# Performance work log

Measured on AMD Instinct MI355X. Metric: run time of the kernel, lower is better.

The kernel has to match this reference:

```python
import jax, jax.numpy as jnp
import numpy as np

N, C, K, KEIG, B, NG, H = 32768, 128, 5, 128, 64, 512, 4
E = 524288
EPS = 1e-5


def setup_inputs() -> dict:
    key = jax.random.key(0)
    ks = iter(jax.random.split(key, 40))
    def nrm(shape, scale):
        return jax.random.normal(next(ks), shape, jnp.float32) * scale
    s = 1.0 / np.sqrt(C)
    return dict(
        x=nrm((N, C), 1.0),
        U=nrm((N, KEIG), 1.0 / np.sqrt(N)),
        Lambda=jax.random.uniform(next(ks), (KEIG,), jnp.float32, 0.0, 2.0),
        lambda_max=jnp.full((1,), 2.0, jnp.float32),
        w_spa1=nrm((C, C), s), b_spa1=jnp.zeros((C,), jnp.float32),
        w_spa2=nrm((C, C), s), b_spa2=jnp.zeros((C,), jnp.float32),
        w_spe1=nrm((C, C), s), b_spe1=jnp.zeros((C,), jnp.float32),
        w_spe2=nrm((C, C), s), b_spe2=jnp.zeros((C,), jnp.float32),
        cheb_w=nrm((K, C, C), s), cheb_b=jnp.zeros((C,), jnp.float32),
        gamma=jnp.ones((1,), jnp.float32),
        w_proj=nrm((C, C), s),
        w_qkv=nrm((C, 3 * C), s), b_qkv=jnp.zeros((3 * C,), jnp.float32),
        w_out=nrm((C, C), s), b_out=jnp.zeros((C,), jnp.float32),
        mlp_w1=nrm((C, 2 * C), s), mlp_b1=jnp.zeros((2 * C,), jnp.float32),
        mlp_w2=nrm((2 * C, C), 1.0 / np.sqrt(2 * C)), mlp_b2=jnp.zeros((C,), jnp.float32),
        bn1_w=jnp.ones((C,), jnp.float32), bn1_b=jnp.zeros((C,), jnp.float32),
        bn2_w=jnp.ones((C,), jnp.float32), bn2_b=jnp.zeros((C,), jnp.float32),
        bn3_w=jnp.ones((C,), jnp.float32), bn3_b=jnp.zeros((C,), jnp.float32),
        edge_index=jax.random.randint(next(ks), (2, E), 0, N, jnp.int64) if jax.config.jax_enable_x64 else jax.random.randint(next(ks), (2, E), 0, N, jnp.int32),
        batch=jnp.repeat(jnp.arange(B), NG),  # 64 graphs of 512 nodes each
    )


def _mlp2(h, w1, b1, w2, b2):
    return jnp.maximum(h @ w1 + b1, 0.0) @ w2 + b2


def _bn(h, w, b):
    # train-mode BatchNorm1d over node dim (biased variance), GPSConv default norm
    mu = h.mean(0)
    var = jnp.mean((h - mu) ** 2, 0)
    return (h - mu) * jax.lax.rsqrt(var + EPS) * w + b


def _cheb(x, src, dst, lam, Ws, bias):
    # L_hat = (2/lambda_max) * (I - D^{-1/2} A D^{-1/2}) - I ; sym normalization
    deg = jax.ops.segment_sum(jnp.ones_like(src, x.dtype), src, num_segments=N)
    dis = jnp.where(deg > 0, 1.0 / jnp.sqrt(deg), 0.0)
    w = dis[src] * dis[dst]  # [E]
    scale = 2.0 / lam
    def lhat(v):
        agg = jax.ops.segment_sum(w[:, None] * v[src], dst, num_segments=N)
        return (scale - 1.0) * v - scale * agg
    Tx0 = x
    out = Tx0 @ Ws[0]
    Tx1 = lhat(Tx0)
    out = out + Tx1 @ Ws[1]
    for k in range(2, K):
        Tx2 = 2.0 * lhat(Tx1) - Tx0
        out = out + Tx2 @ Ws[k]
        Tx0, Tx1 = Tx1, Tx2
    return out + bias


def _mha(xd, w_qkv, b_qkv, w_out, b_out):
    Bq, n, _ = xd.shape
    dh = C // H
    qkv = xd @ w_qkv + b_qkv  # [B,n,3C]
    q, k, v = jnp.split(qkv, 3, axis=-1)
    heads = lambda t: t.reshape(Bq, n, H, dh).transpose(0, 2, 1, 3)
    q, k, v = heads(q), heads(k), heads(v)
    a = jax.nn.softmax(jnp.einsum('bhqd,bhkd->bhqk', q, k) / np.sqrt(dh), axis=-1)
    o = jnp.einsum('bhqk,bhkd->bhqd', a, v).transpose(0, 2, 1, 3).reshape(Bq, n, C)
    return o @ w_out + b_out


def reference(x, U, Lambda, lambda_max,
              w_spa1, b_spa1, w_spa2, b_spa2,
              w_spe1, b_spe1, w_spe2, b_spe2,
              cheb_w, cheb_b, gamma, w_proj,
              w_qkv, b_qkv, w_out, b_out,
              mlp_w1, mlp_b1, mlp_w2, mlp_b2,
              bn1_w, bn1_b, bn2_w, bn2_b, bn3_w, bn3_b,
              edge_index, batch):
    src, dst = edge_index[0], edge_index[1]
    lam = lambda_max[0]
    # ---- SpectralLocalNN (GPSConv local conv branch) ----
    x_sp = _mlp2(x, w_spa1, b_spa1, w_spa2, b_spa2)
    out_local = _cheb(x_sp, src, dst, lam, cheb_w, cheb_b)
    x_spec = _mlp2(x, w_spe1, b_spe1, w_spe2, b_spe2)
    h_proj = x_spec @ w_proj
    s_lam = jnp.exp(-gamma[0] * Lambda ** 2)  # [k_eig]
    out_spectral = U @ (s_lam[:, None] * (U.T @ h_proj))
    h1 = _bn(out_local + out_spectral + x, bn1_w, bn1_b)
    # ---- global attention branch (equal-size graphs -> dense reshape) ----
    xd = x.reshape(B, NG, C)
    h2 = _mha(xd, w_qkv, b_qkv, w_out, b_out).reshape(N, C)
    h2 = _bn(h2 + x, bn2_w, bn2_b)
    # ---- combine + MLP ----
    out = h1 + h2
    out = out + _mlp2(out, mlp_w1, mlp_b1, mlp_w2, mlp_b2)
    return _bn(out, bn3_w, bn3_b)
```

## Files before the change

### kernel.cpp

```cpp
#include <hip/hip_runtime.h>

typedef short bf16x8 __attribute__((ext_vector_type(8)));
typedef short bf16x4 __attribute__((ext_vector_type(4)));
typedef float f32x4 __attribute__((ext_vector_type(4)));

#define DEVI __device__ __forceinline__

constexpr int N   = 32768;
constexpr int C   = 128;
constexpr int E   = 524288;
constexpr float EPSV = 1e-5f;
constexpr int UT_BLOCKS = 128;
constexpr int HB  = 64;
constexpr int EPB = E / HB;
constexpr float QSCALE = 0.17677669529663687f * 1.4426950408889634f;

DEVI float bf2f(ushort u){ return __uint_as_float(((uint)u) << 16); }
DEVI ushort f2bf(float f){
  uint u = __float_as_uint(f);
  return (ushort)((u + 0x7fffu + ((u >> 16) & 1u)) >> 16);
}
DEVI uint cvtpk(float lo, float hi){
  uint r;
  asm("v_cvt_pk_bf16_f32 %0, %1, %2" : "=v"(r) : "v"(lo), "v"(hi));
  return r;
}
DEVI float fexp2(float x){
  float r;
  asm("v_exp_f32 %0, %1" : "=v"(r) : "v"(x));
  return r;
}
DEVI float sane(float v){ if (!(v == v)) return 0.f; return fminf(fmaxf(v, -1e30f), 1e30f); }
DEVI bool mode_fp32(const uint* lmraw){ return (lmraw[0] & 0xffffu) == 0u; }

constexpr int CSZ[28] = {128,1,16384,128,16384,128,16384,128,16384,128,81920,128,
                         1,16384,49152,384,16384,128,32768,256,32768,128,
                         128,128,128,128,128,128};
constexpr int COF[28] = {0,128,192,16576,16704,33088,33216,49600,49728,66112,
                         66240,148160,148288,148352,164736,213888,214272,230656,
                         230784,263552,263808,296576,296704,296832,296960,297088,
                         297216,297344};
constexpr int CAN_SMALL_TOTAL = 297472;

struct CvtArgs { const void* src[28]; };

__global__ __launch_bounds__(256) void convert_small(CvtArgs a, ushort* __restrict__ can,
                                                     const uint* __restrict__ lmraw)
{
  bool f32 = mode_fp32(lmraw);
  int idx = blockIdx.x * 256 + threadIdx.x;
  #pragma unroll 1
  for (int s = 0; s < 28; s++) {
    if (idx < CSZ[s]) {
      ushort v = f32 ? f2bf(((const float*)a.src[s])[idx])
                     : ((const ushort*)a.src[s])[idx];
      can[COF[s] + idx] = v;
      return;
    }
    idx -= CSZ[s];
  }
}

__global__ __launch_bounds__(256) void convert_big(const void* __restrict__ xs,
    const void* __restrict__ Us, ushort* __restrict__ canx, ushort* __restrict__ canu,
    const uint* __restrict__ lmraw)
{
  bool f32 = mode_fp32(lmraw);
  size_t e = ((size_t)blockIdx.x * 256 + threadIdx.x) * 4;
  bool isU = e >= (size_t)N * C;
  size_t off = isU ? e - (size_t)N * C : e;
  const void* src = isU ? Us : xs;
  ushort* dst = isU ? canu : canx;
  ushort4 o;
  if (f32) {
    float4 v = *(const float4*)((const float*)src + off);
    o.x = f2bf(v.x); o.y = f2bf(v.y); o.z = f2bf(v.z); o.w = f2bf(v.w);
  } else {
    o = *(const ushort4*)((const ushort*)src + off);
  }
  *(ushort4*)(dst + off) = o;
}

__global__ __launch_bounds__(1024) void hist_lds(const int* __restrict__ ei,
    int* __restrict__ cei, ushort* __restrict__ part)
{
  __shared__ uint hist[N / 2];
  int t = threadIdx.x;
  int b = blockIdx.x;
  bool i64 = ((ei[1] | ei[3] | ei[5] | ei[7]) == 0);
  size_t j0 = (size_t)b * EPB;
  #pragma unroll
  for (int i = t; i < N / 2; i += 1024) hist[i] = 0u;
  __syncthreads();
  for (int k = t; k < EPB; k += 1024) {
    size_t j = j0 + k;
    int v = (i64 ? ei[2 * j] : ei[j]) & (N - 1);
    cei[j] = v;
    atomicAdd(&hist[v >> 1], 1u << ((v & 1) * 16));
  }
  __syncthreads();
  uint* po = (uint*)(part + (size_t)b * N);
  for (int i = t; i < N / 2; i += 1024) po[i] = hist[i];
}

__global__ __launch_bounds__(256) void reduce_cnt(const ushort* __restrict__ part,
    int* __restrict__ cdt, float* __restrict__ dis)
{
  int d = blockIdx.x * 256 + threadIdx.x;
  int s = 0, tt = 0;
  #pragma unroll 8
  for (int b = 0; b < HB; b++) s  += part[(size_t)b * N + d];
  #pragma unroll 8
  for (int b = 0; b < HB; b++) tt += part[(size_t)(HB + b) * N + d];
  cdt[d] = tt;
  dis[d] = s > 0 ? rsqrtf((float)s) : 0.f;
}

__global__ __launch_bounds__(1024) void scan_kernel(const int* __restrict__ cnt,
                                                    int* __restrict__ row_ptr)
{
  __shared__ int sums[1024];
  int t = threadIdx.x;
  int loc[32]; int s = 0;
  int base = t * 32;
  #pragma unroll
  for (int i = 0; i < 32; i++) { loc[i] = s; s += cnt[base + i]; }
  sums[t] = s;
  __syncthreads();
  for (int off = 1; off < 1024; off <<= 1) {
    int v = (t >= off) ? sums[t - off] : 0;
    __syncthreads();
    sums[t] += v;
    __syncthreads();
  }
  int pre = (t == 0) ? 0 : sums[t - 1];
  #pragma unroll
  for (int i = 0; i < 32; i++) row_ptr[base + i] = pre + loc[i];
}

__global__ __launch_bounds__(256) void off_kernel(const int* __restrict__ rp,
    const ushort* __restrict__ part, int* __restrict__ off2)
{
  int d = blockIdx.x * 256 + threadIdx.x;
  int run = rp[d];
  #pragma unroll 8
  for (int b = 0; b < HB; b++) {
    off2[(size_t)b * N + d] = run;
    run += part[(size_t)(HB + b) * N + d];
  }
}

__global__ __launch_bounds__(1024) void edge_scatter(const int* __restrict__ cei,
    const int* __restrict__ off2, const float* __restrict__ dis,
    int2* __restrict__ ep)
{
  __shared__ int base[N];
  int t = threadIdx.x;
  int b = blockIdx.x;
  for (int i = t; i < N; i += 1024) base[i] = off2[(size_t)b * N + i];
  __syncthreads();
  size_t e0 = (size_t)b * EPB;
  for (int k = t; k < EPB; k += 1024) {
    size_t e = e0 + k;
    int s = cei[e], d = cei[e + E];
    int slot = atomicAdd(&base[d], 1);
    int2 v; v.x = s; v.y = __float_as_int(dis[s] * dis[d]);
    ep[slot] = v;
  }
}

constexpr int WT_SPA1 = 0;
constexpr int WT_SPA2 = 16384;
constexpr int WT_SPE1 = 32768;
constexpr int WT_SPE2 = 49152;
constexpr int WT_PROJ = 65536;
constexpr int WT_CHEB = 81920;
constexpr int WT_QKV  = 163840;
constexpr int WT_WOUT = 212992;
constexpr int WT_MLP1 = 229376;
constexpr int WT_MLP2 = 262144;
constexpr int WT_TOTAL = 294912;

__global__ __launch_bounds__(256) void zero_kernel(int* __restrict__ p, int n)
{
  int i = blockIdx.x * 256 + threadIdx.x;
  if (i < n) p[i] = 0;
}

__global__ __launch_bounds__(256) void transpose_weights(
    const ushort* __restrict__ spa1, const ushort* __restrict__ spa2,
    const ushort* __restrict__ spe1, const ushort* __restrict__ spe2,
    const ushort* __restrict__ proj, const ushort* __restrict__ cheb,
    const ushort* __restrict__ qkv,  const ushort* __restrict__ wout,
    const ushort* __restrict__ mlp1, const ushort* __restrict__ mlp2,
    ushort* __restrict__ wt)
{
  int i = blockIdx.x * 256 + threadIdx.x;
  if (i < 81920) {
    int m = i >> 14, r = i & 16383; int k = r >> 7, n = r & 127;
    const ushort* src = m==0?spa1 : m==1?spa2 : m==2?spe1 : m==3?spe2 : proj;
    wt[m*16384 + n*128 + k] = src[r];
  } else if (i < 163840) {
    int j = i - 81920; int m = j >> 14, r = j & 16383; int k = r >> 7, n = r & 127;
    wt[WT_CHEB + n*640 + m*128 + k] = cheb[j];
  } else if (i < 212992) {
    int j = i - 163840; int k = j / 384, n = j % 384;
    wt[WT_QKV + n*128 + k] = qkv[j];
  } else if (i < 229376) {
    int j = i - 212992; int k = j >> 7, n = j & 127;
    wt[WT_WOUT + n*128 + k] = wout[j];
  } else if (i < 262144) {
    int j = i - 229376; int k = j >> 8, n = j & 255;
    wt[WT_MLP1 + n*128 + k] = mlp1[j];
  } else if (i < WT_TOTAL) {
    int j = i - 262144; int k = j >> 7, n = j & 127;
    wt[WT_MLP2 + n*256 + k] = mlp2[j];
  }
}

template<int K, int COLS, bool RELU, int OMODE, bool BIAS, bool RES, int ASTR, int OSTR, bool QSC>
__global__ __launch_bounds__(256) void gemm_lds(
    const ushort* __restrict__ A, const ushort* __restrict__ WT,
    const ushort* __restrict__ bias, const ushort* __restrict__ res,
    void* __restrict__ outp)
{
  constexpr int NSEG = COLS / 128;
  constexpr int NKC = K / 128;
  constexpr int BP = 136;
  __shared__ ushort Bs[128 * BP];
  int tid = threadIdx.x;
  int lane = tid & 63, wave = tid >> 6;
  int quad = lane >> 4, l16 = lane & 15;
  int seg = (NSEG > 1) ? (blockIdx.x % NSEG) : 0;
  int rb  = (NSEG > 1) ? (blockIdx.x / NSEG) : blockIdx.x;
  int row0 = rb * 64 + wave * 16;
  const ushort* wseg = WT + (size_t)(seg * 128) * K;

  f32x4 acc[8];
  #pragma unroll
  for (int nt = 0; nt < 8; nt++) acc[nt] = (f32x4){0.f, 0.f, 0.f, 0.f};

  for (int kc = 0; kc < NKC; kc++) {
    if (kc) __syncthreads();
    #pragma unroll
    for (int i = tid; i < 2048; i += 256) {
      int col = i >> 4, ko = (i & 15) * 8;
      *(bf16x8*)&Bs[col * BP + ko] =
          *(const bf16x8*)(wseg + (size_t)col * K + kc * 128 + ko);
    }
    __syncthreads();
    bf16x8 a[4];
    const ushort* ap = A + (size_t)(row0 + l16) * ASTR + kc * 128 + quad * 8;
    #pragma unroll
    for (int kk = 0; kk < 4; kk++) a[kk] = *(const bf16x8*)(ap + kk * 32);
    #pragma unroll
    for (int kk = 0; kk < 4; kk++) {
      #pragma unroll
      for (int nt = 0; nt < 8; nt++) {
        bf16x8 b = *(const bf16x8*)(&Bs[(nt * 16 + l16) * BP + kk * 32 + quad * 8]);
        acc[nt] = __builtin_amdgcn_mfma_f32_16x16x32_bf16(a[kk], b, acc[nt], 0, 0, 0);
      }
    }
  }

  #pragma unroll
  for (int nt = 0; nt < 8; nt++) {
    int col = seg * 128 + nt * 16 + l16;
    float bv = 0.f;
    if (BIAS) bv = bf2f(bias[col]);
// ... 165 lines not shown
      #pragma unroll
      for (int nt = 0; nt < 8; nt++) {
        bf16x8 b = *(const bf16x8*)(&Bs[(nt * 16 + l16) * BP + kk * 32 + quad * 8]);
        acc[nt] = __builtin_amdgcn_mfma_f32_16x16x32_bf16(a[kk], b, acc[nt], 0, 0, 0);
      }
    #pragma unroll
    for (int nt = 0; nt < 8; nt++) {
      int col = seg * 128 + nt * 16 + l16;
      float bv = bf2f(B1[col]);
      #pragma unroll
      for (int r = 0; r < 4; r++)
        Hs[(lw + quad * 4 + r) * HP + col] = f2bf(fmaxf(acc[nt][r] + bv, 0.f));
    }
  }
  __syncthreads();

  f32x4 acc2[8];
  #pragma unroll
  for (int nt = 0; nt < 8; nt++) acc2[nt] = (f32x4){0.f, 0.f, 0.f, 0.f};
  for (int kc = 0; kc < 2; kc++) {
    if (kc) __syncthreads();
    for (int i = tid; i < 2048; i += 256) {
      int col = i >> 4, ko = (i & 15) * 8;
      *(bf16x8*)&Bs[col * BP + ko] =
          *(const bf16x8*)(W2 + (size_t)col * 256 + kc * 128 + ko);
    }
    bf16x8 a2[4];
    #pragma unroll
    for (int kk = 0; kk < 4; kk++)
      a2[kk] = *(const bf16x8*)(&Hs[(lw + l16) * HP + kc * 128 + kk * 32 + quad * 8]);
    __syncthreads();
    #pragma unroll
    for (int kk = 0; kk < 4; kk++)
      #pragma unroll
      for (int nt = 0; nt < 8; nt++) {
        bf16x8 b = *(const bf16x8*)(&Bs[(nt * 16 + l16) * BP + kk * 32 + quad * 8]);
        acc2[nt] = __builtin_amdgcn_mfma_f32_16x16x32_bf16(a2[kk], b, acc2[nt], 0, 0, 0);
      }
  }

  #pragma unroll
  for (int nt = 0; nt < 8; nt++) {
    int col = nt * 16 + l16;
    float bv = bf2f(B2[col]);
    #pragma unroll
    for (int r = 0; r < 4; r++) {
      int row = row0 + quad * 4 + r;
      float v = acc2[nt][r] + bv + bf2f(res[(size_t)row * 128 + col]);
      outp[(size_t)row * 128 + col] = v;
    }
  }
}

__global__ __launch_bounds__(256) void spmm_cheb(
    const int* __restrict__ row_ptr, const int2* __restrict__ ep,
    const ushort* __restrict__ v,
    const ushort* __restrict__ txprev, ushort* __restrict__ txout,
    const ushort* __restrict__ lambda_max, int first, int str)
{
  int wave = threadIdx.x >> 6, lane = threadIdx.x & 63;
  int sub = lane >> 4, l16 = lane & 15;
  int d = blockIdx.x * 4 + wave;
  float lm = bf2f(lambda_max[0]);
  float scale = 2.f / lm;
  if (!(scale == scale) || fabsf(scale) > 1e6f) scale = 1.f;
  int beg = row_ptr[d];
  int end = (d == N - 1) ? E : row_ptr[d + 1];
  float acc[8] = {0.f,0.f,0.f,0.f,0.f,0.f,0.f,0.f};
  for (int jb = beg; jb < end; jb += 4) {
    int j = jb + sub;
    bool ok = j < end;
    int2 e2 = ep[ok ? j : beg];
    int s = e2.x & (N - 1);
    float w = ok ? __int_as_float(e2.y) : 0.f;
    bf16x8 vv = *(const bf16x8*)(v + (size_t)s * str + l16 * 8);
    #pragma unroll
    for (int i = 0; i < 8; i++) acc[i] += w * bf2f((ushort)vv[i]);
  }
  #pragma unroll
  for (int i = 0; i < 8; i++) {
    acc[i] += __shfl_xor(acc[i], 16);
    acc[i] += __shfl_xor(acc[i], 32);
  }
  if (sub == 0) {
    bf16x8 vd = *(const bf16x8*)(v + (size_t)d * str + l16 * 8);
    bf16x8 tp;
    if (!first) tp = *(const bf16x8*)(txprev + (size_t)d * str + l16 * 8);
    bf16x8 ov;
    #pragma unroll
    for (int i = 0; i < 8; i++) {
      float r = (scale - 1.f) * bf2f((ushort)vd[i]) - scale * acc[i];
      if (!first) r = 2.f * r - bf2f((ushort)tp[i]);
      ov[i] = (short)f2bf(r);
    }
    *(bf16x8*)(txout + (size_t)d * str + l16 * 8) = ov;
  }
}

__global__ __launch_bounds__(256) void ut_mfma(const ushort* __restrict__ U,
    const ushort* __restrict__ hp, float* __restrict__ parts)
{
  constexpr int RP = 40;
  __shared__ ushort Ut[128 * RP];
  __shared__ ushort Ht[128 * RP];
  int t = threadIdx.x;
  int lane = t & 63, wave = t >> 6;
  int quad = lane >> 4, l16 = lane & 15;

  f32x4 acc[2][8];
  #pragma unroll
  for (int a = 0; a < 2; a++)
    #pragma unroll
    for (int ct = 0; ct < 8; ct++) acc[a][ct] = (f32x4){0.f, 0.f, 0.f, 0.f};

  for (int ch = 0; ch < 8; ch++) {
    int n0 = blockIdx.x * 256 + ch * 32;
    __syncthreads();
    for (int i = t; i < 2048; i += 256) {
      int r2 = i >> 7, c = i & 127;
      uint u0 = U [(size_t)(n0 + r2 * 2) * 128 + c];
      uint u1 = U [(size_t)(n0 + r2 * 2 + 1) * 128 + c];
      *(uint*)&Ut[c * RP + r2 * 2] = (u0 & 0xffffu) | (u1 << 16);
      uint h0 = hp[(size_t)(n0 + r2 * 2) * 128 + c];
      uint h1 = hp[(size_t)(n0 + r2 * 2 + 1) * 128 + c];
      *(uint*)&Ht[c * RP + r2 * 2] = (h0 & 0xffffu) | (h1 << 16);
    }
    __syncthreads();
    bf16x8 bfr[8];
    #pragma unroll
    for (int ct = 0; ct < 8; ct++)
      bfr[ct] = *(const bf16x8*)(&Ht[(ct * 16 + l16) * RP + quad * 8]);
    #pragma unroll
    for (int a = 0; a < 2; a++) {
      int kt = wave * 2 + a;
      bf16x8 af = *(const bf16x8*)(&Ut[(kt * 16 + l16) * RP + quad * 8]);
      #pragma unroll
      for (int ct = 0; ct < 8; ct++)
        acc[a][ct] = __builtin_amdgcn_mfma_f32_16x16x32_bf16(af, bfr[ct], acc[a][ct], 0, 0, 0);
    }
  }

  float* po = parts + (size_t)blockIdx.x * 16384;
  #pragma unroll
  for (int a = 0; a < 2; a++) {
    int kt = wave * 2 + a;
    #pragma unroll
    for (int ct = 0; ct < 8; ct++)
      #pragma unroll
      for (int r = 0; r < 4; r++)
        po[(kt * 16 + quad * 4 + r) * 128 + ct * 16 + l16] = acc[a][ct][r];
  }
}

__global__ __launch_bounds__(256) void reduce_mt(const float* __restrict__ parts,
    const ushort* __restrict__ Lambda, const ushort* __restrict__ gamma,
    ushort* __restrict__ MT)
{
  int e = blockIdx.x * 256 + threadIdx.x;
  int keig = e >> 7, c = e & 127;
  float s = 0.f;
  for (int p = 0; p < UT_BLOCKS; p++) s += parts[(size_t)p * 16384 + e];
  float g = bf2f(gamma[0]);
  float lam = bf2f(Lambda[keig]);
  float sl = __expf(-g * lam * lam);
  MT[c * 128 + keig] = f2bf(sl * s);
}

__global__ __launch_bounds__(256) void bn_stats(const float* __restrict__ h,
                                                float* __restrict__ stats)
{
  int c = threadIdx.x & 127, half = threadIdx.x >> 7;
  int r0 = blockIdx.x * 128 + half;
  float s = 0.f, s2 = 0.f;
  for (int i = 0; i < 64; i++) {
    float v = sane(h[(size_t)(r0 + i * 2) * 128 + c]);
    s += v; s2 += v * v;
  }
  atomicAdd(&stats[c], s);
  atomicAdd(&stats[128 + c], s2);
}

__global__ __launch_bounds__(256) void bn_apply(const float* __restrict__ h,
    const float* __restrict__ st, const ushort* __restrict__ gw,
    const ushort* __restrict__ gb, const ushort* __restrict__ add,
    void* __restrict__ out, const uint* __restrict__ lmraw, int final_out)
{
  size_t e = ((size_t)blockIdx.x * 256 + threadIdx.x) * 4;
  int c0 = (int)(e & 127);
  float4 hv = *(const float4*)(h + e);
  float xv[4] = {sane(hv.x), sane(hv.y), sane(hv.z), sane(hv.w)};
  float addv[4] = {0.f, 0.f, 0.f, 0.f};
  if (add) {
    ushort4 av = *(const ushort4*)(add + e);
    addv[0] = bf2f(av.x); addv[1] = bf2f(av.y);
    addv[2] = bf2f(av.z); addv[3] = bf2f(av.w);
  }
  float r[4];
  #pragma unroll
  for (int j = 0; j < 4; j++) {
    int c = c0 + j;
    float mu = st[c] * (1.f / 32768.f);
    float var = fmaxf(st[128 + c] * (1.f / 32768.f) - mu * mu, 0.f);
    r[j] = (xv[j] - mu) * rsqrtf(var + EPSV) * bf2f(gw[c]) + bf2f(gb[c]) + addv[j];
  }
  if (final_out && mode_fp32(lmraw)) {
    float4 o4; o4.x = r[0]; o4.y = r[1]; o4.z = r[2]; o4.w = r[3];
    *(float4*)((float*)out + e) = o4;
  } else {
    ushort4 o;
    o.x = f2bf(r[0]); o.y = f2bf(r[1]); o.z = f2bf(r[2]); o.w = f2bf(r[3]);
    *(ushort4*)((ushort*)out + e) = o;
  }
}

__global__ __launch_bounds__(512) void attn_mfma(const ushort* __restrict__ qkv,
                                                 ushort* __restrict__ attn)
{
  constexpr int VP = 516;
  constexpr int KP = 40;
  __shared__ ushort Kt[512 * KP];
  __shared__ ushort Vt[32 * VP];
  int b = blockIdx.x;
  int g = b >> 3, hh = (b >> 1) & 3, half = b & 1;
  int lane = threadIdx.x & 63, wave = threadIdx.x >> 6;
  int quad = lane >> 4, l16 = lane & 15;
  const ushort* base = qkv + (size_t)g * 512 * 384;

  for (int i = threadIdx.x; i < 512 * 4; i += 512) {
    int key = i >> 2, c8 = (i & 3) * 8;
    *(bf16x8*)&Kt[key * KP + c8] =
        *(const bf16x8*)(base + (size_t)key * 384 + 128 + hh * 32 + c8);
  }
  for (int i = threadIdx.x; i < 256 * 8; i += 512) {
    int kp = i >> 3, d4 = (i & 7) * 4;
    const ushort* va = base + (size_t)(2 * kp) * 384 + 256 + hh * 32 + d4;
    ushort4 a = *(const ushort4*)va;
    ushort4 c = *(const ushort4*)(va + 384);
    *(uint*)&Vt[(d4 + 0) * VP + 2 * kp] = (uint)a.x | ((uint)c.x << 16);
    *(uint*)&Vt[(d4 + 1) * VP + 2 * kp] = (uint)a.y | ((uint)c.y << 16);
    *(uint*)&Vt[(d4 + 2) * VP + 2 * kp] = (uint)a.z | ((uint)c.z << 16);
    *(uint*)&Vt[(d4 + 3) * VP + 2 * kp] = (uint)a.w | ((uint)c.w << 16);
  }
  __syncthreads();

  int q0 = half * 256 + wave * 32;
  bf16x8 qf[2];
  #pragma unroll
  for (int i = 0; i < 2; i++)
    qf[i] = *(const bf16x8*)(base + (size_t)(q0 + i * 16 + l16) * 384 + hh * 32 + quad * 8);

  f32x4 O[2][2];
  #pragma unroll
  for (int dt = 0; dt < 2; dt++)
    #pragma unroll
    for (int i = 0; i < 2; i++) O[dt][i] = (f32x4){0.f, 0.f, 0.f, 0.f};
  float lsum[2] = {0.f, 0.f};

  union PU { uint u[4]; bf16x8 v; };
  union VU { uint2 a[2]; bf16x8 v; };

  for (int kt2 = 0; kt2 < 16; kt2++) {
    int k0 = kt2 * 32;
    bf16x8 kfA = *(const bf16x8*)&Kt[(k0 + l16) * KP + quad * 8];
    bf16x8 kfB = *(const bf16x8*)&Kt[(k0 + 16 + l16) * KP + quad * 8];
// ... 68 lines not shown
constexpr size_t OFF_PARTS = 87 * MB;

extern "C" void kernel_launch(void* const* d_in, const int* in_sizes, int n_in,
                              void* d_out, int out_size, void* d_ws, size_t ws_size,
                              hipStream_t stream) {
  (void)in_sizes; (void)n_in; (void)out_size; (void)ws_size;
  const uint* lmraw = (const uint*)d_in[3];
  const int*  ei    = (const int*)d_in[30];

  char* W = (char*)d_ws;
  ushort* wt    = (ushort*)(W + OFF_WT);
  int*    cdt   = (int*)(W + OFF_CDT);
  int*    rp    = (int*)(W + OFF_RP);
  float*  dis   = (float*)(W + OFF_DIS);
  ushort* MT    = (ushort*)(W + OFF_MT);
  float*  stats = (float*)(W + OFF_STATS);
  int*    cei   = (int*)(W + OFF_CEI);
  int2*   ep    = (int2*)(W + OFF_EP);
  ushort* part  = (ushort*)(W + OFF_PARTH);
  int*    off2  = (int*)(W + OFF_OFF2);
  ushort* canx  = (ushort*)(W + OFF_CANX);
  ushort* canu  = (ushort*)(W + OFF_CANU);
  ushort* cs    = (ushort*)(W + OFF_CANS);
  float*  F1    = (float*)(W + OFF_F1);
  ushort* hproj = (ushort*)(W + OFF_HPROJ);
  ushort* Tbig  = (ushort*)(W + OFF_TBIG);
  ushort* qkvb  = (ushort*)(W + OFF_TBIG);
  float*  parts = (float*)(W + OFF_PARTS);
  ushort* attnb = (ushort*)(W + OFF_PARTS);
  ushort* h1    = (ushort*)(W + OFF_CANU);
  ushort* comb  = (ushort*)(W + OFF_CANX);

  const ushort* cLambda = cs + COF[0];
  const ushort* cLmx    = cs + COF[1];
  const ushort* cBspa1  = cs + COF[3];
  const ushort* cBspa2  = cs + COF[5];
  const ushort* cBspe1  = cs + COF[7];
  const ushort* cBspe2  = cs + COF[9];
  const ushort* cChebB  = cs + COF[11];
  const ushort* cGam    = cs + COF[12];
  const ushort* cBqkv   = cs + COF[15];
  const ushort* cBout   = cs + COF[17];
  const ushort* cMb1    = cs + COF[19];
  const ushort* cMb2    = cs + COF[21];
  const ushort* cBn1w   = cs + COF[22];
  const ushort* cBn1b   = cs + COF[23];
  const ushort* cBn2w   = cs + COF[24];
  const ushort* cBn2b   = cs + COF[25];
  const ushort* cBn3w   = cs + COF[26];
  const ushort* cBn3b   = cs + COF[27];

  const ushort* NUL = nullptr;

  zero_kernel<<<3, 256, 0, stream>>>((int*)(W + OFF_STATS), 768);

  CvtArgs ca;
  ca.src[0]  = d_in[2];  ca.src[1]  = d_in[3];  ca.src[2]  = d_in[4];
  ca.src[3]  = d_in[5];  ca.src[4]  = d_in[6];  ca.src[5]  = d_in[7];
  ca.src[6]  = d_in[8];  ca.src[7]  = d_in[9];  ca.src[8]  = d_in[10];
  ca.src[9]  = d_in[11]; ca.src[10] = d_in[12]; ca.src[11] = d_in[13];
  ca.src[12] = d_in[14]; ca.src[13] = d_in[15]; ca.src[14] = d_in[16];
  ca.src[15] = d_in[17]; ca.src[16] = d_in[18]; ca.src[17] = d_in[19];
  ca.src[18] = d_in[20]; ca.src[19] = d_in[21]; ca.src[20] = d_in[22];
  ca.src[21] = d_in[23]; ca.src[22] = d_in[24]; ca.src[23] = d_in[25];
  ca.src[24] = d_in[26]; ca.src[25] = d_in[27]; ca.src[26] = d_in[28];
  ca.src[27] = d_in[29];
  convert_small<<<(CAN_SMALL_TOTAL + 255) / 256, 256, 0, stream>>>(ca, cs, lmraw);
  convert_big<<<(2 * N * C / 4) / 256, 256, 0, stream>>>(d_in[0], d_in[1], canx, canu, lmraw);

  transpose_weights<<<1152, 256, 0, stream>>>(cs + COF[2], cs + COF[4], cs + COF[6],
      cs + COF[8], cs + COF[13], cs + COF[10], cs + COF[14], cs + COF[16],
      cs + COF[18], cs + COF[20], wt);

  hist_lds<<<2 * HB, 1024, 0, stream>>>(ei, cei, part);
  reduce_cnt<<<N / 256, 256, 0, stream>>>(part, cdt, dis);
  scan_kernel<<<1, 1024, 0, stream>>>(cdt, rp);
  off_kernel<<<N / 256, 256, 0, stream>>>(rp, part, off2);
  edge_scatter<<<HB, 1024, 0, stream>>>(cei, off2, dis, ep);

  dim3 g1(512), g3(1536), bb(256);
  gemm_chain<false, 640><<<g1, bb, 0, stream>>>(canx, wt + WT_SPA1, cBspa1,
      wt + WT_SPA2, cBspa2, NUL, Tbig);
  gemm_chain<true, 128><<<g1, bb, 0, stream>>>(canx, wt + WT_SPE1, cBspe1,
      wt + WT_SPE2, cBspe2, wt + WT_PROJ, hproj);

  ut_mfma<<<UT_BLOCKS, 256, 0, stream>>>(canu, hproj, parts);
  reduce_mt<<<64, 256, 0, stream>>>(parts, cLambda, cGam, MT);

  spmm_cheb<<<N / 4, 256, 0, stream>>>(rp, ep, Tbig,       NUL,        Tbig + 128, cLmx, 1, 640);
  spmm_cheb<<<N / 4, 256, 0, stream>>>(rp, ep, Tbig + 128, Tbig,       Tbig + 256, cLmx, 0, 640);
  spmm_cheb<<<N / 4, 256, 0, stream>>>(rp, ep, Tbig + 256, Tbig + 128, Tbig + 384, cLmx, 0, 640);
  spmm_cheb<<<N / 4, 256, 0, stream>>>(rp, ep, Tbig + 384, Tbig + 256, Tbig + 512, cLmx, 0, 640);
  gemm_lds<640,128,false,1,true ,false,640,128,false><<<g1, bb, 0, stream>>>(Tbig, wt + WT_CHEB, cChebB, NUL, F1);

  gemm_lds<128,128,false,2,false,true ,128,128,false><<<g1, bb, 0, stream>>>(canu, MT, NUL, canx, F1);
  bn_stats<<<256, 256, 0, stream>>>(F1, stats);
  bn_apply<<<(N * C) / 1024, 256, 0, stream>>>(F1, stats, cBn1w, cBn1b, NUL, h1, lmraw, 0);

  gemm_lds<128,384,false,0,true ,false,128,384,true ><<<g3, bb, 0, stream>>>(canx, wt + WT_QKV, cBqkv, NUL, qkvb);
  attn_mfma<<<512, 512, 0, stream>>>(qkvb, attnb);
  gemm_lds<128,128,false,1,true ,true ,128,128,false><<<g1, bb, 0, stream>>>(attnb, wt + WT_WOUT, cBout, canx, F1);
  bn_stats<<<256, 256, 0, stream>>>(F1, stats + 256);
  bn_apply<<<(N * C) / 1024, 256, 0, stream>>>(F1, stats + 256, cBn2w, cBn2b, h1, comb, lmraw, 0);

  gemm_mlp<<<g1, bb, 0, stream>>>(comb, wt + WT_MLP1, cMb1, wt + WT_MLP2, cMb2, comb, F1);
  bn_stats<<<256, 256, 0, stream>>>(F1, stats + 512);
  bn_apply<<<(N * C) / 1024, 256, 0, stream>>>(F1, stats + 512, cBn3w, cBn3b, NUL, d_out, lmraw, 1);
}
```

Measured before the change: 538.3 us.

## Merge prep kernels and use cooperative grid-sync for Chebyshev SpMM and BatchNorm

Folds zeroing, small/big input conversion and weight transposition into one prep kernel, with the transposes now reading raw inputs directly. The four Chebyshev SpMM launches become one cooperative kernel that processes 8 rows per wave, prefetches the next edge, and calls grid.sync between orders. Each bn_stats/bn_apply pair becomes one cooperative kernel that syncs the grid after the atomic stats. This targets launch overhead and inter-kernel gaps, but the fixed grid of 1024 blocks gives the SpMM fewer waves in flight to hide gather latency.

```diff
diff --git a/kernel.cpp b/kernel.cpp
--- a/kernel.cpp
+++ b/kernel.cpp
@@ -1,4 +1,7 @@
 #include <hip/hip_runtime.h>
+#include <hip/hip_cooperative_groups.h>
+
+namespace cg = cooperative_groups;
 
 typedef short bf16x8 __attribute__((ext_vector_type(8)));
 typedef short bf16x4 __attribute__((ext_vector_type(4)));
@@ -41,133 +44,6 @@
                          230784,263552,263808,296576,296704,296832,296960,297088,
                          297216,297344};
 constexpr int CAN_SMALL_TOTAL = 297472;
-
-struct CvtArgs { const void* src[28]; };
-
-__global__ __launch_bounds__(256) void convert_small(CvtArgs a, ushort* __restrict__ can,
-                                                     const uint* __restrict__ lmraw)
-{
-  bool f32 = mode_fp32(lmraw);
-  int idx = blockIdx.x * 256 + threadIdx.x;
-  #pragma unroll 1
-  for (int s = 0; s < 28; s++) {
-    if (idx < CSZ[s]) {
-      ushort v = f32 ? f2bf(((const float*)a.src[s])[idx])
-                     : ((const ushort*)a.src[s])[idx];
-      can[COF[s] + idx] = v;
-      return;
-    }
-    idx -= CSZ[s];
-  }
-}
-
-__global__ __launch_bounds__(256) void convert_big(const void* __restrict__ xs,
-    const void* __restrict__ Us, ushort* __restrict__ canx, ushort* __restrict__ canu,
-    const uint* __restrict__ lmraw)
-{
-  bool f32 = mode_fp32(lmraw);
-  size_t e = ((size_t)blockIdx.x * 256 + threadIdx.x) * 4;
-  bool isU = e >= (size_t)N * C;
-  size_t off = isU ? e - (size_t)N * C : e;
-  const void* src = isU ? Us : xs;
-  ushort* dst = isU ? canu : canx;
-  ushort4 o;
-  if (f32) {
-    float4 v = *(const float4*)((const float*)src + off);
-    o.x = f2bf(v.x); o.y = f2bf(v.y); o.z = f2bf(v.z); o.w = f2bf(v.w);
-  } else {
-    o = *(const ushort4*)((const ushort*)src + off);
-  }
-  *(ushort4*)(dst + off) = o;
-}
-
-__global__ __launch_bounds__(1024) void hist_lds(const int* __restrict__ ei,
-    int* __restrict__ cei, ushort* __restrict__ part)
-{
-  __shared__ uint hist[N / 2];
-  int t = threadIdx.x;
-  int b = blockIdx.x;
-  bool i64 = ((ei[1] | ei[3] | ei[5] | ei[7]) == 0);
-  size_t j0 = (size_t)b * EPB;
-  #pragma unroll
-  for (int i = t; i < N / 2; i += 1024) hist[i] = 0u;
-  __syncthreads();
-  for (int k = t; k < EPB; k += 1024) {
-    size_t j = j0 + k;
-    int v = (i64 ? ei[2 * j] : ei[j]) & (N - 1);
-    cei[j] = v;
-    atomicAdd(&hist[v >> 1], 1u << ((v & 1) * 16));
-  }
-  __syncthreads();
-  uint* po = (uint*)(part + (size_t)b * N);
-  for (int i = t; i < N / 2; i += 1024) po[i] = hist[i];
-}
-
-__global__ __launch_bounds__(256) void reduce_cnt(const ushort* __restrict__ part,
-    int* __restrict__ cdt, float* __restrict__ dis)
-{
-  int d = blockIdx.x * 256 + threadIdx.x;
-  int s = 0, tt = 0;
-  #pragma unroll 8
-  for (int b = 0; b < HB; b++) s  += part[(size_t)b * N + d];
-  #pragma unroll 8
-  for (int b = 0; b < HB; b++) tt += part[(size_t)(HB + b) * N + d];
-  cdt[d] = tt;
-  dis[d] = s > 0 ? rsqrtf((float)s) : 0.f;
-}
-
-__global__ __launch_bounds__(1024) void scan_kernel(const int* __restrict__ cnt,
-                                                    int* __restrict__ row_ptr)
-{
-  __shared__ int sums[1024];
-  int t = threadIdx.x;
-  int loc[32]; int s = 0;
-  int base = t * 32;
-  #pragma unroll
-  for (int i = 0; i < 32; i++) { loc[i] = s; s += cnt[base + i]; }
-  sums[t] = s;
-  __syncthreads();
-  for (int off = 1; off < 1024; off <<= 1) {
-    int v = (t >= off) ? sums[t - off] : 0;
-    __syncthreads();
-    sums[t] += v;
-    __syncthreads();
-  }
-  int pre = (t == 0) ? 0 : sums[t - 1];
-  #pragma unroll
-  for (int i = 0; i < 32; i++) row_ptr[base + i] = pre + loc[i];
-}
-
-__global__ __launch_bounds__(256) void off_kernel(const int* __restrict__ rp,
-    const ushort* __restrict__ part, int* __restrict__ off2)
-{
-  int d = blockIdx.x * 256 + threadIdx.x;
-  int run = rp[d];
-  #pragma unroll 8
-  for (int b = 0; b < HB; b++) {
-    off2[(size_t)b * N + d] = run;
-    run += part[(size_t)(HB + b) * N + d];
-  }
-}
-
-__global__ __launch_bounds__(1024) void edge_scatter(const int* __restrict__ cei,
-    const int* __restrict__ off2, const float* __restrict__ dis,
-    int2* __restrict__ ep)
-{
-  __shared__ int base[N];
-  int t = threadIdx.x;
-  int b = blockIdx.x;
-  for (int i = t; i < N; i += 1024) base[i] = off2[(size_t)b * N + i];
-  __syncthreads();
-  size_t e0 = (size_t)b * EPB;
-  for (int k = t; k < EPB; k += 1024) {
-    size_t e = e0 + k;
-    int s = cei[e], d = cei[e + E];
-    int slot = atomicAdd(&base[d], 1);
-    int2 v; v.x = s; v.y = __float_as_int(dis[s] * dis[d]);
-    ep[slot] = v;
-  }
-}
 
 constexpr int WT_SPA1 = 0;
 constexpr int WT_SPA2 = 16384;
@@ -181,40 +57,154 @@
 constexpr int WT_MLP2 = 262144;
 constexpr int WT_TOTAL = 294912;
 
-__global__ __launch_bounds__(256) void zero_kernel(int* __restrict__ p, int n)
-{
-  int i = blockIdx.x * 256 + threadIdx.x;
-  if (i < n) p[i] = 0;
-}
-
-__global__ __launch_bounds__(256) void transpose_weights(
-    const ushort* __restrict__ spa1, const ushort* __restrict__ spa2,
-    const ushort* __restrict__ spe1, const ushort* __restrict__ spe2,
-    const ushort* __restrict__ proj, const ushort* __restrict__ cheb,
-    const ushort* __restrict__ qkv,  const ushort* __restrict__ wout,
-    const ushort* __restrict__ mlp1, const ushort* __restrict__ mlp2,
-    ushort* __restrict__ wt)
-{
-  int i = blockIdx.x * 256 + threadIdx.x;
-  if (i < 81920) {
-    int m = i >> 14, r = i & 16383; int k = r >> 7, n = r & 127;
-    const ushort* src = m==0?spa1 : m==1?spa2 : m==2?spe1 : m==3?spe2 : proj;
-    wt[m*16384 + n*128 + k] = src[r];
-  } else if (i < 163840) {
-    int j = i - 81920; int m = j >> 14, r = j & 16383; int k = r >> 7, n = r & 127;
-    wt[WT_CHEB + n*640 + m*128 + k] = cheb[j];
-  } else if (i < 212992) {
-    int j = i - 163840; int k = j / 384, n = j % 384;
-    wt[WT_QKV + n*128 + k] = qkv[j];
-  } else if (i < 229376) {
-    int j = i - 212992; int k = j >> 7, n = j & 127;
-    wt[WT_WOUT + n*128 + k] = wout[j];
-  } else if (i < 262144) {
-    int j = i - 229376; int k = j >> 8, n = j & 255;
-    wt[WT_MLP1 + n*128 + k] = mlp1[j];
-  } else if (i < WT_TOTAL) {
-    int j = i - 262144; int k = j >> 7, n = j & 127;
-    wt[WT_MLP2 + n*256 + k] = mlp2[j];
+struct CvtArgs { const void* src[28]; };
+
+DEVI ushort cvt_elem(const void* p, int j, bool f32){
+  return f32 ? f2bf(((const float*)p)[j]) : ((const ushort*)p)[j];
+}
+
+__global__ __launch_bounds__(256) void prep_all(CvtArgs a,
+    const void* __restrict__ xs, const void* __restrict__ Us,
+    ushort* __restrict__ canx, ushort* __restrict__ canu,
+    ushort* __restrict__ cs, ushort* __restrict__ wt,
+    int* __restrict__ zp, const uint* __restrict__ lmraw)
+{
+  bool f32 = mode_fp32(lmraw);
+  int b = blockIdx.x, tid = threadIdx.x;
+  if (b < 8192) {
+    size_t e = ((size_t)b * 256 + tid) * 4;
+    bool isU = e >= (size_t)N * C;
+    size_t off = isU ? e - (size_t)N * C : e;
+    const void* src = isU ? Us : xs;
+    ushort* dst = isU ? canu : canx;
+    ushort4 o;
+    if (f32) {
+      float4 v = *(const float4*)((const float*)src + off);
+      o.x = f2bf(v.x); o.y = f2bf(v.y); o.z = f2bf(v.z); o.w = f2bf(v.w);
+    } else {
+      o = *(const ushort4*)((const ushort*)src + off);
+    }
+    *(ushort4*)(dst + off) = o;
+  } else if (b < 9354) {
+    int idx = (b - 8192) * 256 + tid;
+    #pragma unroll 1
+    for (int s = 0; s < 28; s++) {
+      if (idx < CSZ[s]) { cs[COF[s] + idx] = cvt_elem(a.src[s], idx, f32); return; }
+      idx -= CSZ[s];
+    }
+  } else if (b < 10506) {
+    int i = (b - 9354) * 256 + tid;
+    if (i < 81920) {
+      int m = i >> 14, r = i & 16383; int k = r >> 7, n = r & 127;
+      const void* src = m==0?a.src[2] : m==1?a.src[4] : m==2?a.src[6] : m==3?a.src[8] : a.src[13];
+      wt[m*16384 + n*128 + k] = cvt_elem(src, r, f32);
+    } else if (i < 163840) {
+      int j = i - 81920; int m = j >> 14, r = j & 16383; int k = r >> 7, n = r & 127;
+      wt[WT_CHEB + n*640 + m*128 + k] = cvt_elem(a.src[10], j, f32);
+    } else if (i < 212992) {
+      int j = i - 163840; int k = j / 384, n = j % 384;
+      wt[WT_QKV + n*128 + k] = cvt_elem(a.src[14], j, f32);
+    } else if (i < 229376) {
+      int j = i - 212992; int k = j >> 7, n = j & 127;
+      wt[WT_WOUT + n*128 + k] = cvt_elem(a.src[16], j, f32);
+    } else if (i < 262144) {
+      int j = i - 229376; int k = j >> 8, n = j & 255;
+      wt[WT_MLP1 + n*128 + k] = cvt_elem(a.src[18], j, f32);
+    } else if (i < WT_TOTAL) {
+      int j = i - 262144; int k = j >> 7, n = j & 127;
+      wt[WT_MLP2 + n*256 + k] = cvt_elem(a.src[20], j, f32);
+    }
+  } else {
+    int i = (b - 10506) * 256 + tid;
+    if (i < 768) zp[i] = 0;
+  }
+}
+
+__global__ __launch_bounds__(1024) void hist_lds(const int* __restrict__ ei,
+    int* __restrict__ cei, ushort* __restrict__ part)
+{
+  __shared__ uint hist[N / 2];
+  int t = threadIdx.x;
+  int b = blockIdx.x;
+  bool i64 = ((ei[1] | ei[3] | ei[5] | ei[7]) == 0);
+  size_t j0 = (size_t)b * EPB;
+  #pragma unroll
+  for (int i = t; i < N / 2; i += 1024) hist[i] = 0u;
+  __syncthreads();
+  for (int k = t; k < EPB; k += 1024) {
+    size_t j = j0 + k;
+    int v = (i64 ? ei[2 * j] : ei[j]) & (N - 1);
+    cei[j] = v;
+    atomicAdd(&hist[v >> 1], 1u << ((v & 1) * 16));
+  }
+  __syncthreads();
+  uint* po = (uint*)(part + (size_t)b * N);
+  for (int i = t; i < N / 2; i += 1024) po[i] = hist[i];
+}
+
+__global__ __launch_bounds__(256) void reduce_cnt(const ushort* __restrict__ part,
+    int* __restrict__ cdt, float* __restrict__ dis)
+{
+  int d = blockIdx.x * 256 + threadIdx.x;
+  int s = 0, tt = 0;
+  #pragma unroll 8
+  for (int b = 0; b < HB; b++) s  += part[(size_t)b * N + d];
+  #pragma unroll 8
+  for (int b = 0; b < HB; b++) tt += part[(size_t)(HB + b) * N + d];
+  cdt[d] = tt;
+  dis[d] = s > 0 ? rsqrtf((float)s) : 0.f;
+}
+
+__global__ __launch_bounds__(1024) void scan_kernel(const int* __restrict__ cnt,
+                                                    int* __restrict__ row_ptr)
+{
+  __shared__ int sums[1024];
+  int t = threadIdx.x;
+  int loc[32]; int s = 0;
+  int base = t * 32;
+  #pragma unroll
+  for (int i = 0; i < 32; i++) { loc[i] = s; s += cnt[base + i]; }
+  sums[t] = s;
+  __syncthreads();
+  for (int off = 1; off < 1024; off <<= 1) {
+    int v = (t >= off) ? sums[t - off] : 0;
+    __syncthreads();
+    sums[t] += v;
+    __syncthreads();
+  }
+  int pre = (t == 0) ? 0 : sums[t - 1];
+  #pragma unroll
+  for (int i = 0; i < 32; i++) row_ptr[base + i] = pre + loc[i];
+}
+
+__global__ __launch_bounds__(256) void off_kernel(const int* __restrict__ rp,
+    const ushort* __restrict__ part, int* __restrict__ off2)
+{
+  int d = blockIdx.x * 256 + threadIdx.x;
+  int run = rp[d];
+  #pragma unroll 8
+  for (int b = 0; b < HB; b++) {
+    off2[(size_t)b * N + d] = run;
+    run += part[(size_t)(HB + b) * N + d];
+  }
+}
+
+__global__ __launch_bounds__(1024) void edge_scatter(const int* __restrict__ cei,
+    const int* __restrict__ off2, const float* __restrict__ dis,
+    int2* __restrict__ ep)
+{
+  __shared__ int base[N];
+  int t = threadIdx.x;
+  int b = blockIdx.x;
+  for (int i = t; i < N; i += 1024) base[i] = off2[(size_t)b * N + i];
+  __syncthreads();
+  size_t e0 = (size_t)b * EPB;
+  for (int k = t; k < EPB; k += 1024) {
+    size_t e = e0 + k;
+    int s = cei[e], d = cei[e + E];
+    int slot = atomicAdd(&base[d], 1);
+    int2 v; v.x = s; v.y = __float_as_int(dis[s] * dis[d]);
+    ep[slot] = v;
   }
 }
 
@@ -486,48 +476,61 @@
   }
 }
 
-__global__ __launch_bounds__(256) void spmm_cheb(
-    const int* __restrict__ row_ptr, const int2* __restrict__ ep,
-    const ushort* __restrict__ v,
-    const ushort* __restrict__ txprev, ushort* __restrict__ txout,
-    const ushort* __restrict__ lambda_max, int first, int str)
-{
+__global__ __launch_bounds__(256) void spmm_coop(
+    const int* __restrict__ rp, const int2* __restrict__ ep,
+    ushort* __restrict__ Tbig, const ushort* __restrict__ lambda_max)
+{
+  cg::grid_group grid = cg::this_grid();
   int wave = threadIdx.x >> 6, lane = threadIdx.x & 63;
   int sub = lane >> 4, l16 = lane & 15;
-  int d = blockIdx.x * 4 + wave;
+  int wg = blockIdx.x * 4 + wave;
   float lm = bf2f(lambda_max[0]);
   float scale = 2.f / lm;
   if (!(scale == scale) || fabsf(scale) > 1e6f) scale = 1.f;
-  int beg = row_ptr[d];
-  int end = (d == N - 1) ? E : row_ptr[d + 1];
-  float acc[8] = {0.f,0.f,0.f,0.f,0.f,0.f,0.f,0.f};
-  for (int jb = beg; jb < end; jb += 4) {
-    int j = jb + sub;
-    bool ok = j < end;
-    int2 e2 = ep[ok ? j : beg];
-    int s = e2.x & (N - 1);
-    float w = ok ? __int_as_float(e2.y) : 0.f;
-    bf16x8 vv = *(const bf16x8*)(v + (size_t)s * str + l16 * 8);
-    #pragma unroll
-    for (int i = 0; i < 8; i++) acc[i] += w * bf2f((ushort)vv[i]);
-  }
-  #pragma unroll
-  for (int i = 0; i < 8; i++) {
-    acc[i] += __shfl_xor(acc[i], 16);
-    acc[i] += __shfl_xor(acc[i], 32);
-  }
-  if (sub == 0) {
-    bf16x8 vd = *(const bf16x8*)(v + (size_t)d * str + l16 * 8);
-    bf16x8 tp;
-    if (!first) tp = *(const bf16x8*)(txprev + (size_t)d * str + l16 * 8);
-    bf16x8 ov;
-    #pragma unroll
-    for (int i = 0; i < 8; i++) {
-      float r = (scale - 1.f) * bf2f((ushort)vd[i]) - scale * acc[i];
-      if (!first) r = 2.f * r - bf2f((ushort)tp[i]);
-      ov[i] = (short)f2bf(r);
-    }
-    *(bf16x8*)(txout + (size_t)d * str + l16 * 8) = ov;
+
+  for (int k = 0; k < 4; k++) {
+    const ushort* v  = Tbig + 128 * k;
+    const ushort* tp = Tbig + 128 * (k - 1);
+    ushort* out      = Tbig + 128 * (k + 1);
+    bool first = (k == 0);
+    for (int n = 0; n < 8; n++) {
+      int d = wg * 8 + n;
+      int beg = rp[d];
+      int end = (d == N - 1) ? E : rp[d + 1];
+      float acc[8] = {0.f,0.f,0.f,0.f,0.f,0.f,0.f,0.f};
+      int j0 = beg + sub;
+      int2 e2 = ep[j0 < end ? j0 : 0];
+      for (int jb = beg; jb < end; jb += 4) {
+        int jn = jb + 4 + sub;
+        int2 en = ep[jn < end ? jn : 0];
+        bool ok = (jb + sub) < end;
+        int s = e2.x & (N - 1);
+        float w = ok ? __int_as_float(e2.y) : 0.f;
+        bf16x8 vv = *(const bf16x8*)(v + (size_t)s * 640 + l16 * 8);
+        #pragma unroll
+        for (int i = 0; i < 8; i++) acc[i] += w * bf2f((ushort)vv[i]);
+        e2 = en;
+      }
+      #pragma unroll
+      for (int i = 0; i < 8; i++) {
+        acc[i] += __shfl_xor(acc[i], 16);
+        acc[i] += __shfl_xor(acc[i], 32);
+      }
+      if (sub == 0) {
+        bf16x8 vd = *(const bf16x8*)(v + (size_t)d * 640 + l16 * 8);
+        bf16x8 tpv;
+        if (!first) tpv = *(const bf16x8*)(tp + (size_t)d * 640 + l16 * 8);
+        bf16x8 ov;
+        #pragma unroll
+        for (int i = 0; i < 8; i++) {
+          float r = (scale - 1.f) * bf2f((ushort)vd[i]) - scale * acc[i];
+          if (!first) r = 2.f * r - bf2f((ushort)tpv[i]);
+          ov[i] = (short)f2bf(r);
+        }
+        *(bf16x8*)(out + (size_t)d * 640 + l16 * 8) = ov;
+      }
+    }
+    grid.sync();
   }
 }
 
@@ -600,9 +603,12 @@
   MT[c * 128 + keig] = f2bf(sl * s);
 }
 
-__global__ __launch_bounds__(256) void bn_stats(const float* __restrict__ h,
-                                                float* __restrict__ stats)
-{
+__global__ __launch_bounds__(256) void bn_coop(const float* __restrict__ h,
+    float* __restrict__ st, const ushort* __restrict__ gw,
+    const ushort* __restrict__ gb, const ushort* __restrict__ add,
+    void* __restrict__ out, const uint* __restrict__ lmraw, int final_out)
+{
+  cg::grid_group grid = cg::this_grid();
   int c = threadIdx.x & 127, half = threadIdx.x >> 7;
   int r0 = blockIdx.x * 128 + half;
   float s = 0.f, s2 = 0.f;
@@ -610,40 +616,38 @@
     float v = sane(h[(size_t)(r0 + i * 2) * 128 + c]);
     s += v; s2 += v * v;
   }
-  atomicAdd(&stats[c], s);
-  atomicAdd(&stats[128 + c], s2);
-}
-
-__global__ __launch_bounds__(256) void bn_apply(const float* __restrict__ h,
-    const float* __restrict__ st, const ushort* __restrict__ gw,
-    const ushort* __restrict__ gb, const ushort* __restrict__ add,
-    void* __restrict__ out, const uint* __restrict__ lmraw, int final_out)
-{
-  size_t e = ((size_t)blockIdx.x * 256 + threadIdx.x) * 4;
-  int c0 = (int)(e & 127);
-  float4 hv = *(const float4*)(h + e);
-  float xv[4] = {sane(hv.x), sane(hv.y), sane(hv.z), sane(hv.w)};
-  float addv[4] = {0.f, 0.f, 0.f, 0.f};
-  if (add) {
-    ushort4 av = *(const ushort4*)(add + e);
-    addv[0] = bf2f(av.x); addv[1] = bf2f(av.y);
-    addv[2] = bf2f(av.z); addv[3] = bf2f(av.w);
-  }
-  float r[4];
-  #pragma unroll
-  for (int j = 0; j < 4; j++) {
-    int c = c0 + j;
-    float mu = st[c] * (1.f / 32768.f);
-    float var = fmaxf(st[128 + c] * (1.f / 32768.f) - mu * mu, 0.f);
-    r[j] = (xv[j] - mu) * rsqrtf(var + EPSV) * bf2f(gw[c]) + bf2f(gb[c]) + addv[j];
-  }
-  if (final_out && mode_fp32(lmraw)) {
-    float4 o4; o4.x = r[0]; o4.y = r[1]; o4.z = r[2]; o4.w = r[3];
-    *(float4*)((float*)out + e) = o4;
-  } else {
-    ushort4 o;
-    o.x = f2bf(r[0]); o.y = f2bf(r[1]); o.z = f2bf(r[2]); o.w = f2bf(r[3]);
-    *(ushort4*)((ushort*)out + e) = o;
+  atomicAdd(&st[c], s);
+  atomicAdd(&st[128 + c], s2);
+  grid.sync();
+
+  bool f32out = final_out && mode_fp32(lmraw);
+  for (int it = 0; it < 16; it++) {
+    size_t e = (size_t)blockIdx.x * 16384 + ((size_t)it * 256 + threadIdx.x) * 4;
+    int c0 = (int)(e & 127);
+    float4 hv = *(const float4*)(h + e);
+    float xv[4] = {sane(hv.x), sane(hv.y), sane(hv.z), sane(hv.w)};
+    float addv[4] = {0.f, 0.f, 0.f, 0.f};
+    if (add) {
+      ushort4 av = *(const ushort4*)(add + e);
+      addv[0] = bf2f(av.x); addv[1] = bf2f(av.y);
+      addv[2] = bf2f(av.z); addv[3] = bf2f(av.w);
+    }
+    float r[4];
+    #pragma unroll
+    for (int j = 0; j < 4; j++) {
+      int cc = c0 + j;
+      float mu = st[cc] * (1.f / 32768.f);
+      float var = fmaxf(st[128 + cc] * (1.f / 32768.f) - mu * mu, 0.f);
+      r[j] = (xv[j] - mu) * rsqrtf(var + EPSV) * bf2f(gw[cc]) + bf2f(gb[cc]) + addv[j];
+    }
+    if (f32out) {
+      float4 o4; o4.x = r[0]; o4.y = r[1]; o4.z = r[2]; o4.w = r[3];
+      *(float4*)((float*)out + e) = o4;
+    } else {
+      ushort4 o;
+      o.x = f2bf(r[0]); o.y = f2bf(r[1]); o.z = f2bf(r[2]); o.w = f2bf(r[3]);
+      *(ushort4*)((ushort*)out + e) = o;
+    }
   }
 }
 
@@ -818,8 +822,6 @@
 
   const ushort* NUL = nullptr;
 
-  zero_kernel<<<3, 256, 0, stream>>>((int*)(W + OFF_STATS), 768);
-
   CvtArgs ca;
   ca.src[0]  = d_in[2];  ca.src[1]  = d_in[3];  ca.src[2]  = d_in[4];
   ca.src[3]  = d_in[5];  ca.src[4]  = d_in[6];  ca.src[5]  = d_in[7];
@@ -831,12 +833,8 @@
   ca.src[21] = d_in[23]; ca.src[22] = d_in[24]; ca.src[23] = d_in[25];
   ca.src[24] = d_in[26]; ca.src[25] = d_in[27]; ca.src[26] = d_in[28];
   ca.src[27] = d_in[29];
-  convert_small<<<(CAN_SMALL_TOTAL + 255) / 256, 256, 0, stream>>>(ca, cs, lmraw);
-  convert_big<<<(2 * N * C / 4) / 256, 256, 0, stream>>>(d_in[0], d_in[1], canx, canu, lmraw);
-
-  transpose_weights<<<1152, 256, 0, stream>>>(cs + COF[2], cs + COF[4], cs + COF[6],
-      cs + COF[8], cs + COF[13], cs + COF[10], cs + COF[14], cs + COF[16],
-      cs + COF[18], cs + COF[20], wt);
+  prep_all<<<10509, 256, 0, stream>>>(ca, d_in[0], d_in[1], canx, canu, cs, wt,
+                                      (int*)(W + OFF_STATS), lmraw);
 
   hist_lds<<<2 * HB, 1024, 0, stream>>>(ei, cei, part);
   reduce_cnt<<<N / 256, 256, 0, stream>>>(part, cdt, dis);
@@ -853,23 +851,43 @@
   ut_mfma<<<UT_BLOCKS, 256, 0, stream>>>(canu, hproj, parts);
   reduce_mt<<<64, 256, 0, stream>>>(parts, cLambda, cGam, MT);
 
-  spmm_cheb<<<N / 4, 256, 0, stream>>>(rp, ep, Tbig,       NUL,        Tbig + 128, cLmx, 1, 640);
-  spmm_cheb<<<N / 4, 256, 0, stream>>>(rp, ep, Tbig + 128, Tbig,       Tbig + 256, cLmx, 0, 640);
-  spmm_cheb<<<N / 4, 256, 0, stream>>>(rp, ep, Tbig + 256, Tbig + 128, Tbig + 384, cLmx, 0, 640);
-  spmm_cheb<<<N / 4, 256, 0, stream>>>(rp, ep, Tbig + 384, Tbig + 256, Tbig + 512, cLmx, 0, 640);
+  {
+    const int* a0 = rp; const int2* a1 = ep; ushort* a2 = Tbig;
+    const ushort* a3 = cLmx;
+    void* args[] = {(void*)&a0, (void*)&a1, (void*)&a2, (void*)&a3};
+    hipLaunchCooperativeKernel(spmm_coop, dim3(1024), dim3(256), args, 0, stream);
+  }
   gemm_lds<640,128,false,1,true ,false,640,128,false><<<g1, bb, 0, stream>>>(Tbig, wt + WT_CHEB, cChebB, NUL, F1);
 
   gemm_lds<128,128,false,2,false,true ,128,128,false><<<g1, bb, 0, stream>>>(canu, MT, NUL, canx, F1);
-  bn_stats<<<256, 256, 0, stream>>>(F1, stats);
-  bn_apply<<<(N * C) / 1024, 256, 0, stream>>>(F1, stats, cBn1w, cBn1b, NUL, h1, lmraw, 0);
+  {
+    const float* a0 = F1; float* a1 = stats; const ushort* a2 = cBn1w;
+    const ushort* a3 = cBn1b; const ushort* a4 = NUL; void* a5 = h1;
+    const uint* a6 = lmraw; int a7 = 0;
+    void* args[] = {(void*)&a0,(void*)&a1,(void*)&a2,(void*)&a3,(void*)&a4,
+                    (void*)&a5,(void*)&a6,(void*)&a7};
+    hipLaunchCooperativeKernel(bn_coop, dim3(256), dim3(256), args, 0, stream);
+  }
 
   gemm_lds<128,384,false,0,true ,false,128,384,true ><<<g3, bb, 0, stream>>>(canx, wt + WT_QKV, cBqkv, NUL, qkvb);
   attn_mfma<<<512, 512, 0, stream>>>(qkvb, attnb);
   gemm_lds<128,128,false,1,true ,true ,128,128,false><<<g1, bb, 0, stream>>>(attnb, wt + WT_WOUT, cBout, canx, F1);
-  bn_stats<<<256, 256, 0, stream>>>(F1, stats + 256);
-  bn_apply<<<(N * C) / 1024, 256, 0, stream>>>(F1, stats + 256, cBn2w, cBn2b, h1, comb, lmraw, 0);
+  {
+    const float* a0 = F1; float* a1 = stats + 256; const ushort* a2 = cBn2w;
+    const ushort* a3 = cBn2b; const ushort* a4 = h1; void* a5 = comb;
+    const uint* a6 = lmraw; int a7 = 0;
+    void* args[] = {(void*)&a0,(void*)&a1,(void*)&a2,(void*)&a3,(void*)&a4,
+                    (void*)&a5,(void*)&a6,(void*)&a7};
+    hipLaunchCooperativeKernel(bn_coop, dim3(256), dim3(256), args, 0, stream);
+  }
 
   gemm_mlp<<<g1, bb, 0, stream>>>(comb, wt + WT_MLP1, cMb1, wt + WT_MLP2, cMb2, comb, F1);
-  bn_stats<<<256, 256, 0, stream>>>(F1, stats + 512);
-  bn_apply<<<(N * C) / 1024, 256, 0, stream>>>(F1, stats + 512, cBn3w, cBn3b, NUL, d_out, lmraw, 1);
-}
+  {
+    const float* a0 = F1; float* a1 = stats + 512; const ushort* a2 = cBn3w;
+    const ushort* a3 = cBn3b; const ushort* a4 = NUL; void* a5 = d_out;
+    const uint* a6 = lmraw; int a7 = 1;
+    void* args[] = {(void*)&a0,(void*)&a1,(void*)&a2,(void*)&a3,(void*)&a4,
+                    (void*)&a5,(void*)&a6,(void*)&a7};
+    hipLaunchCooperativeKernel(bn_coop, dim3(256), dim3(256), args, 0, stream);
+  }
+}
```

After: 1.211 ms. 125% more time.
